# Kernel tuning notes

Measured on AMD Instinct MI355X. Metric: run time of the kernel, lower is better.

The kernel has to match this reference:

```python
import jax, jax.numpy as jnp
import numpy as np
from jax import lax

WINDOW = 11
C1 = (0.01 * 1) ** 2
C2 = (0.03 * 1) ** 2


def setup_inputs() -> dict:
    key = jax.random.key(0)
    kx, ky = jax.random.split(key)
    x = jax.random.uniform(kx, (8, 3, 512, 512), dtype=jnp.float32)
    y = jax.random.uniform(ky, (8, 3, 512, 512), dtype=jnp.float32)
    return {"x": x, "y": y}


def _window_sum(a):
    # sum over every overlapping WINDOW x WINDOW patch (stride 1, valid)
    return lax.reduce_window(a, 0.0, lax.add,
                             (1, 1, WINDOW, WINDOW),
                             (1, 1, 1, 1), 'VALID')


def reference(x, y):
    # x, y: [B, C, H, W] images in [0, 1]
    n = float(WINDOW * WINDOW)
    sx = _window_sum(x)
    sy = _window_sum(y)
    sxx = _window_sum(x * x)
    syy = _window_sum(y * y)
    sxy = _window_sum(x * y)
    mx = sx / n
    my = sy / n
    # unbiased variance / covariance (matches torch var(unbiased=True) and
    # the bessel-corrected covariance in the original)
    vx = (sxx - n * mx * mx) / (n - 1.0)
    vy = (syy - n * my * my) / (n - 1.0)
    cov = (sxy - n * mx * my) / (n - 1.0)
    ssim = (2.0 * mx * my + C1) * (2.0 * cov + C2) / (
        (mx * mx + my * my + C1) * (vx + vy + C2))
    # original averages over windows (dim 0) and channels (dim 2) -> per-batch
    return (1.0 - ssim.mean(axis=(1, 2, 3))) / 2.0
```

## Files before the change

kernel.cpp:

```cpp
#include <hip/hip_runtime.h>

#define WINDOW 11
#define H 512
#define W 512
#define OH 502
#define OW 502
#define NCH 3
#define BATCH 8
#define RSTRIPE 11
#define NSTRIPES 46
#define NGRP 5
#define GRPW 118
#define WAVES_PER_IMG (NSTRIPES * NGRP)
#define NWAVES (BATCH * NCH * WAVES_PER_IMG)
#define WAVES_PER_BATCH (NCH * WAVES_PER_IMG)
#define NXCD 8
#define CHUNK (NWAVES / NXCD)

#define NPIX_PER_BATCH (3.0f * 502.0f * 502.0f)

typedef float v2f __attribute__((ext_vector_type(2)));

template <int CTRL, int RM>
__device__ __forceinline__ float scan_step(float x) {
    int s = __builtin_amdgcn_update_dpp(0, __builtin_bit_cast(int, x),
                                        CTRL, RM, 0xf, false);
    return x + __builtin_bit_cast(float, s);
}
__device__ __forceinline__ float wave_iscan(float x) {
    x = scan_step<0x111, 0xf>(x);
    x = scan_step<0x112, 0xf>(x);
    x = scan_step<0x114, 0xf>(x);
    x = scan_step<0x118, 0xf>(x);
    x = scan_step<0x142, 0xa>(x);
    x = scan_step<0x143, 0xc>(x);
    return x;
}

__global__ __launch_bounds__(64) void ssim_main(const float* __restrict__ x,
                                                const float* __restrict__ y,
                                                float* __restrict__ partials) {
    const int lane = threadIdx.x & 63;

    const int wg    = blockIdx.x;
    const int w_lin = (wg % NXCD) * CHUNK + wg / NXCD;

    const int img = w_lin / WAVES_PER_IMG;
    const int rem = w_lin % WAVES_PER_IMG;
    const int grp = rem / NSTRIPES;
    const int rs  = rem % NSTRIPES;

    const int i0 = rs * RSTRIPE;
    const int i1 = min(i0 + RSTRIPE, OH);
    const int cstart = grp * GRPW;
    const int outw   = min(GRPW, OW - cstart);
    const int c0 = min(cstart + 2 * lane, W - 2);
    const bool tapActive = (2 * lane < outw);

    const float* __restrict__ xc = x + (size_t)img * H * W + c0;
    const float* __restrict__ yc = y + (size_t)img * H * W + c0;

    v2f fx[11], fy[11];
    v2f Qx = 0.f, Qy = 0.f, Qz = 0.f, Qw = 0.f;
#pragma unroll
    for (int r = 0; r < WINDOW; ++r) {
        v2f a = *(const v2f*)(xc + (size_t)(i0 + r) * W);
        v2f b = *(const v2f*)(yc + (size_t)(i0 + r) * W);
        fx[r] = a; fy[r] = b;
        Qx += a;
        Qy += b;
        Qz += a * a + b * b;
        Qw += a * b;
    }

    v2f nxA, nyA, nxB, nyB;
#define LDROW(j, nx, ny) do {                                        \
        int jc_ = min((j), H - 1);                                   \
        nx = *(const v2f*)(xc + (size_t)jc_ * W);                    \
        ny = *(const v2f*)(yc + (size_t)jc_ * W);                    \
    } while (0)

#define SLIDE(u, nx, ny) do {                                         \
        Qx += nx - fx[u];                                             \
        Qy += ny - fy[u];                                             \
        Qz += nx * nx + ny * ny - fx[u] * fx[u] - fy[u] * fy[u];      \
        Qw += nx * ny - fx[u] * fy[u];                                \
        fx[u] = nx; fy[u] = ny;                                       \
    } while (0)

    float acc = 0.f;

#define COMPUTE(rowActive) do {                                               \
        float Tx = Qx.x + Qx.y, Ty = Qy.x + Qy.y;                             \
        float Tz = Qz.x + Qz.y, Tw = Qw.x + Qw.y;                             \
        float Sx = wave_iscan(Tx), Sy = wave_iscan(Ty);                       \
        float Sz = wave_iscan(Tz), Sw = wave_iscan(Tw);                       \
        int src = lane + 5;                                                   \
        float Ax = __shfl(Sx, src, 64), Ay = __shfl(Sy, src, 64);             \
        float Az = __shfl(Sz, src, 64), Aw = __shfl(Sw, src, 64);             \
        float Bx = __shfl(Qx.y, src, 64), By = __shfl(Qy.y, src, 64);         \
        float Bz = __shfl(Qz.y, src, 64), Bw = __shfl(Qw.y, src, 64);         \
        v2f Wx = {Ax - Bx - Sx + Tx, Ax - Sx + Qx.y};                         \
        v2f Wy = {Ay - By - Sy + Ty, Ay - Sy + Qy.y};                         \
        v2f Wz = {Az - Bz - Sz + Tz, Az - Sz + Qz.y};                         \
        v2f Ww = {Aw - Bw - Sw + Tw, Aw - Sw + Qw.y};                         \
                             \
        v2f mx  = Wx * (1.0f / 121.0f);                                       \
        v2f my  = Wy * (1.0f / 121.0f);                                       \
        v2f mxy = mx * my;                                                    \
        v2f m2  = mx * mx + my * my;                                          \
        v2f cov = (Ww - 121.0f * mxy) * (1.0f / 120.0f);                      \
        v2f vv  = (Wz - 121.0f * m2)  * (1.0f / 120.0f);                      \
        v2f num = (2.0f * mxy + 1e-4f) * (2.0f * cov + 9e-4f);                \
        v2f den = (m2 + 1e-4f) * (vv + 9e-4f);                                \
        float r = num.x * __builtin_amdgcn_rcpf(den.x)                        \
                + num.y * __builtin_amdgcn_rcpf(den.y);                       \
        acc += (tapActive & (rowActive)) ? r : 0.f;                           \
    } while (0)

    LDROW(i0 + WINDOW,     nxA, nyA);
    LDROW(i0 + WINDOW + 1, nxB, nyB);
#pragma unroll
    for (int u = 0; u < 11; ++u) {
        const int i = i0 + u;
        COMPUTE(i < i1);
        if ((u & 1) == 0) {
            SLIDE(u, nxA, nyA);
            LDROW(i + WINDOW + 2, nxA, nyA);
        } else {
            SLIDE(u, nxB, nyB);
            LDROW(i + WINDOW + 2, nxB, nyB);
        }
    }

    for (int off = 32; off > 0; off >>= 1)
        acc += __shfl_down(acc, off, 64);
    if (lane == 0) partials[w_lin] = acc;
}

__global__ __launch_bounds__(64) void ssim_reduce(const float* __restrict__ partials,
                                                  float* __restrict__ out) {
    const int b    = blockIdx.x;
    const int lane = threadIdx.x & 63;
    float s = 0.f;
    for (int k = lane; k < WAVES_PER_BATCH; k += 64)
        s += partials[b * WAVES_PER_BATCH + k];
    for (int off = 32; off > 0; off >>= 1)
        s += __shfl_down(s, off, 64);
    if (lane == 0)
        out[b] = (1.0f - s / NPIX_PER_BATCH) * 0.5f;
}

extern "C" void kernel_launch(void* const* d_in, const int* in_sizes, int n_in,
                              void* d_out, int out_size, void* d_ws, size_t ws_size,
                              hipStream_t stream) {
    const float* x = (const float*)d_in[0];
    const float* y = (const float*)d_in[1];
    float* out      = (float*)d_out;
    float* partials = (float*)d_ws;

    ssim_main<<<NWAVES, 64, 0, stream>>>(x, y, partials);
    ssim_reduce<<<BATCH, 64, 0, stream>>>(partials, out);
}
```

Before: 29.60 us.

## Process full-width rows per wave with 8 columns per lane and 2-row stripes

Each wave now covers a whole 512-wide row, with every lane loading 8 contiguous columns as two float4 loads. A stripe is now 2 output rows instead of 11 rows across 5 column groups. Horizontal window sums use a local prefix plus a wave scan and shuffles from lanes +1 and +2. This removes the overlapping column-group halos and gives wider, coalesced loads. The cost is re-reading the 11-row vertical window for every 2 output rows, which is roughly 6x more vertical reload traffic (mostly cache hits), plus more waves and higher register use.

```diff
diff --git a/kernel.cpp b/kernel.cpp
--- a/kernel.cpp
+++ b/kernel.cpp
@@ -7,11 +7,9 @@
 #define OW 502
 #define NCH 3
 #define BATCH 8
-#define RSTRIPE 11
-#define NSTRIPES 46
-#define NGRP 5
-#define GRPW 118
-#define WAVES_PER_IMG (NSTRIPES * NGRP)
+#define RSTRIPE 2
+#define NSTRIPES 251
+#define WAVES_PER_IMG NSTRIPES
 #define NWAVES (BATCH * NCH * WAVES_PER_IMG)
 #define WAVES_PER_BATCH (NCH * WAVES_PER_IMG)
 #define NXCD 8
@@ -19,6 +17,7 @@
 
 #define NPIX_PER_BATCH (3.0f * 502.0f * 502.0f)
 
+typedef float v4f __attribute__((ext_vector_type(4)));
 typedef float v2f __attribute__((ext_vector_type(2)));
 
 template <int CTRL, int RM>
@@ -46,92 +45,110 @@
     const int w_lin = (wg % NXCD) * CHUNK + wg / NXCD;
 
     const int img = w_lin / WAVES_PER_IMG;
-    const int rem = w_lin % WAVES_PER_IMG;
-    const int grp = rem / NSTRIPES;
-    const int rs  = rem % NSTRIPES;
+    const int rs  = w_lin % WAVES_PER_IMG;
+    const int r0  = 2 * rs;
 
-    const int i0 = rs * RSTRIPE;
-    const int i1 = min(i0 + RSTRIPE, OH);
-    const int cstart = grp * GRPW;
-    const int outw   = min(GRPW, OW - cstart);
-    const int c0 = min(cstart + 2 * lane, W - 2);
-    const bool tapActive = (2 * lane < outw);
-
+    const int c0 = 8 * lane;
     const float* __restrict__ xc = x + (size_t)img * H * W + c0;
     const float* __restrict__ yc = y + (size_t)img * H * W + c0;
 
-    v2f fx[11], fy[11];
-    v2f Qx = 0.f, Qy = 0.f, Qz = 0.f, Qw = 0.f;
+    const bool mp0 = (c0     <= 500);
+    const bool mp1 = (c0 + 2 <= 500);
+    const bool mp2 = (c0 + 4 <= 500);
+    const bool mp3 = (c0 + 6 <= 500);
+
+    const int l1 = lane + 1, l2 = lane + 2;
+
+    v4f Qx0 = 0.f, Qx1 = 0.f, Qy0 = 0.f, Qy1 = 0.f;
+    v4f Qz0 = 0.f, Qz1 = 0.f, Qw0 = 0.f, Qw1 = 0.f;
+    v4f ka0, ka1, kb0, kb1;
+
+#define ACC(a0, a1, b0, b1) do {                                      \
+        Qx0 += a0; Qx1 += a1;                                         \
+        Qy0 += b0; Qy1 += b1;                                         \
+        Qz0 += a0 * a0 + b0 * b0; Qz1 += a1 * a1 + b1 * b1;           \
+        Qw0 += a0 * b0;           Qw1 += a1 * b1;                     \
+    } while (0)
+
 #pragma unroll
     for (int r = 0; r < WINDOW; ++r) {
-        v2f a = *(const v2f*)(xc + (size_t)(i0 + r) * W);
-        v2f b = *(const v2f*)(yc + (size_t)(i0 + r) * W);
-        fx[r] = a; fy[r] = b;
-        Qx += a;
-        Qy += b;
-        Qz += a * a + b * b;
-        Qw += a * b;
+        v4f a0 = *(const v4f*)(xc + (size_t)(r0 + r) * W);
+        v4f a1 = *(const v4f*)(xc + (size_t)(r0 + r) * W + 4);
+        v4f b0 = *(const v4f*)(yc + (size_t)(r0 + r) * W);
+        v4f b1 = *(const v4f*)(yc + (size_t)(r0 + r) * W + 4);
+        if (r == 0) { ka0 = a0; ka1 = a1; kb0 = b0; kb1 = b1; }
+        ACC(a0, a1, b0, b1);
     }
-
-    v2f nxA, nyA, nxB, nyB;
-#define LDROW(j, nx, ny) do {                                        \
-        int jc_ = min((j), H - 1);                                   \
-        nx = *(const v2f*)(xc + (size_t)jc_ * W);                    \
-        ny = *(const v2f*)(yc + (size_t)jc_ * W);                    \
-    } while (0)
-
-#define SLIDE(u, nx, ny) do {                                         \
-        Qx += nx - fx[u];                                             \
-        Qy += ny - fy[u];                                             \
-        Qz += nx * nx + ny * ny - fx[u] * fx[u] - fy[u] * fy[u];      \
-        Qw += nx * ny - fx[u] * fy[u];                                \
-        fx[u] = nx; fy[u] = ny;                                       \
-    } while (0)
 
     float acc = 0.f;
 
-#define COMPUTE(rowActive) do {                                               \
-        float Tx = Qx.x + Qx.y, Ty = Qy.x + Qy.y;                             \
-        float Tz = Qz.x + Qz.y, Tw = Qw.x + Qw.y;                             \
-        float Sx = wave_iscan(Tx), Sy = wave_iscan(Ty);                       \
-        float Sz = wave_iscan(Tz), Sw = wave_iscan(Tw);                       \
-        int src = lane + 5;                                                   \
-        float Ax = __shfl(Sx, src, 64), Ay = __shfl(Sy, src, 64);             \
-        float Az = __shfl(Sz, src, 64), Aw = __shfl(Sw, src, 64);             \
-        float Bx = __shfl(Qx.y, src, 64), By = __shfl(Qy.y, src, 64);         \
-        float Bz = __shfl(Qz.y, src, 64), Bw = __shfl(Qw.y, src, 64);         \
-        v2f Wx = {Ax - Bx - Sx + Tx, Ax - Sx + Qx.y};                         \
-        v2f Wy = {Ay - By - Sy + Ty, Ay - Sy + Qy.y};                         \
-        v2f Wz = {Az - Bz - Sz + Tz, Az - Sz + Qz.y};                         \
-        v2f Ww = {Aw - Bw - Sw + Tw, Aw - Sw + Qw.y};                         \
-                             \
-        v2f mx  = Wx * (1.0f / 121.0f);                                       \
-        v2f my  = Wy * (1.0f / 121.0f);                                       \
-        v2f mxy = mx * my;                                                    \
-        v2f m2  = mx * mx + my * my;                                          \
-        v2f cov = (Ww - 121.0f * mxy) * (1.0f / 120.0f);                      \
-        v2f vv  = (Wz - 121.0f * m2)  * (1.0f / 120.0f);                      \
-        v2f num = (2.0f * mxy + 1e-4f) * (2.0f * cov + 9e-4f);                \
-        v2f den = (m2 + 1e-4f) * (vv + 9e-4f);                                \
-        float r = num.x * __builtin_amdgcn_rcpf(den.x)                        \
-                + num.y * __builtin_amdgcn_rcpf(den.y);                       \
-        acc += (tapActive & (rowActive)) ? r : 0.f;                           \
+#define QWIN(Q0, Q1, w0, w1, w2, w3, w4, w5, w6, w7) do {             \
+        float p0 = Q0.x, p1 = p0 + Q0.y, p2 = p1 + Q0.z;              \
+        float p3 = p2 + Q0.w, p4 = p3 + Q1.x, p5 = p4 + Q1.y;         \
+        float p6 = p5 + Q1.z, T = p6 + Q1.w;                          \
+        float S = wave_iscan(T);                                      \
+        float E = S - T;                                              \
+        float s0 = E + p0, s1 = E + p1, s2 = E + p2, s3 = E + p3;     \
+        float s4 = E + p4, s5 = E + p5, s6 = E + p6;                  \
+        float r1s2 = __shfl(s2, l1, 64), r1s3 = __shfl(s3, l1, 64);   \
+        float r1s4 = __shfl(s4, l1, 64), r1s5 = __shfl(s5, l1, 64);   \
+        float r1s6 = __shfl(s6, l1, 64), r1s7 = __shfl(S,  l1, 64);   \
+        float r2s0 = __shfl(s0, l2, 64), r2s1 = __shfl(s1, l2, 64);   \
+        w0 = r1s2 - E;  w1 = r1s3 - s0;                               \
+        w2 = r1s4 - s1; w3 = r1s5 - s2;                               \
+        w4 = r1s6 - s3; w5 = r1s7 - s4;                               \
+        w6 = r2s0 - s5; w7 = r2s1 - s6;                               \
     } while (0)
 
-    LDROW(i0 + WINDOW,     nxA, nyA);
-    LDROW(i0 + WINDOW + 1, nxB, nyB);
-#pragma unroll
-    for (int u = 0; u < 11; ++u) {
-        const int i = i0 + u;
-        COMPUTE(i < i1);
-        if ((u & 1) == 0) {
-            SLIDE(u, nxA, nyA);
-            LDROW(i + WINDOW + 2, nxA, nyA);
-        } else {
-            SLIDE(u, nxB, nyB);
-            LDROW(i + WINDOW + 2, nxB, nyB);
-        }
+#define SSIM_PAIR(mask, WxP, WyP, WzP, WwP) do {                      \
+        v2f mx  = WxP * (1.0f / 121.0f);                              \
+        v2f my  = WyP * (1.0f / 121.0f);                              \
+        v2f mxy = mx * my;                                            \
+        v2f m2  = mx * mx + my * my;                                  \
+        v2f cov = (WwP - 121.0f * mxy) * (1.0f / 120.0f);             \
+        v2f vv  = (WzP - 121.0f * m2)  * (1.0f / 120.0f);             \
+        v2f num = (2.0f * mxy + 1e-4f) * (2.0f * cov + 9e-4f);        \
+        v2f den = (m2 + 1e-4f) * (vv + 9e-4f);                        \
+        float r = num.x * __builtin_amdgcn_rcpf(den.x)                \
+                + num.y * __builtin_amdgcn_rcpf(den.y);               \
+        acc += (mask) ? r : 0.f;                                      \
+    } while (0)
+
+#define COMPUTE() do {                                                        \
+        float wx0,wx1,wx2,wx3,wx4,wx5,wx6,wx7;                                \
+        float wy0,wy1,wy2,wy3,wy4,wy5,wy6,wy7;                                \
+        float wz0,wz1,wz2,wz3,wz4,wz5,wz6,wz7;                                \
+        float ww0,ww1,ww2,ww3,ww4,ww5,ww6,ww7;                                \
+        QWIN(Qx0,Qx1, wx0,wx1,wx2,wx3,wx4,wx5,wx6,wx7);                       \
+        QWIN(Qy0,Qy1, wy0,wy1,wy2,wy3,wy4,wy5,wy6,wy7);                       \
+        QWIN(Qz0,Qz1, wz0,wz1,wz2,wz3,wz4,wz5,wz6,wz7);                       \
+        QWIN(Qw0,Qw1, ww0,ww1,ww2,ww3,ww4,ww5,ww6,ww7);                       \
+        { v2f Wx={wx0,wx1}, Wy={wy0,wy1}, Wz={wz0,wz1}, Ww={ww0,ww1};         \
+          SSIM_PAIR(mp0, Wx, Wy, Wz, Ww); }                                   \
+        { v2f Wx={wx2,wx3}, Wy={wy2,wy3}, Wz={wz2,wz3}, Ww={ww2,ww3};         \
+          SSIM_PAIR(mp1, Wx, Wy, Wz, Ww); }                                   \
+        { v2f Wx={wx4,wx5}, Wy={wy4,wy5}, Wz={wz4,wz5}, Ww={ww4,ww5};         \
+          SSIM_PAIR(mp2, Wx, Wy, Wz, Ww); }                                   \
+        { v2f Wx={wx6,wx7}, Wy={wy6,wy7}, Wz={wz6,wz7}, Ww={ww6,ww7};         \
+          SSIM_PAIR(mp3, Wx, Wy, Wz, Ww); }                                   \
+    } while (0)
+
+    COMPUTE();
+
+    {
+        v4f na0 = *(const v4f*)(xc + (size_t)(r0 + WINDOW) * W);
+        v4f na1 = *(const v4f*)(xc + (size_t)(r0 + WINDOW) * W + 4);
+        v4f nb0 = *(const v4f*)(yc + (size_t)(r0 + WINDOW) * W);
+        v4f nb1 = *(const v4f*)(yc + (size_t)(r0 + WINDOW) * W + 4);
+        Qx0 += na0 - ka0; Qx1 += na1 - ka1;
+        Qy0 += nb0 - kb0; Qy1 += nb1 - kb1;
+        Qz0 += na0 * na0 + nb0 * nb0 - ka0 * ka0 - kb0 * kb0;
+        Qz1 += na1 * na1 + nb1 * nb1 - ka1 * ka1 - kb1 * kb1;
+        Qw0 += na0 * nb0 - ka0 * kb0;
+        Qw1 += na1 * nb1 - ka1 * kb1;
     }
+
+    COMPUTE();
 
     for (int off = 32; off > 0; off >>= 1)
         acc += __shfl_down(acc, off, 64);
```

Measured after the change: 27.33 us. 1.08x faster.

## Stage all stripe rows into LDS via async global_load_lds with staged waits

Applied to the files above, without the earlier changes.

Replaces the register-held sliding window of direct global v2f loads with asynchronous global-to-LDS loads of all 21 rows per stripe issued up front. Each row step then waits on a decreasing vmcnt and reads the new and old rows from LDS. The aim is to keep every load in flight at once and release register pressure from the fx/fy arrays. In exchange it adds LDS traffic, uses about 21KB of LDS per 64-thread block, which may limit occupancy, and relies on per-lane dword global_load_lds ordering semantics.

```diff
diff --git a/kernel.cpp b/kernel.cpp
--- a/kernel.cpp
+++ b/kernel.cpp
@@ -21,6 +21,17 @@
 
 typedef float v2f __attribute__((ext_vector_type(2)));
 
+#define GL_LDS(gsrc, ldst)                                                    \
+    __builtin_amdgcn_global_load_lds(                                         \
+        (const __attribute__((address_space(1))) unsigned int*)(gsrc),        \
+        (__attribute__((address_space(3))) unsigned int*)(ldst), 4, 0, 0)
+
+template <int N>
+__device__ __forceinline__ void vwait() {
+    asm volatile("s_waitcnt vmcnt(%0)" :: "i"(N) : "memory");
+    __builtin_amdgcn_sched_barrier(0);
+}
+
 template <int CTRL, int RM>
 __device__ __forceinline__ float scan_step(float x) {
     int s = __builtin_amdgcn_update_dpp(0, __builtin_bit_cast(int, x),
@@ -40,6 +51,9 @@
 __global__ __launch_bounds__(64) void ssim_main(const float* __restrict__ x,
                                                 const float* __restrict__ y,
                                                 float* __restrict__ partials) {
+    __shared__ float LX[21][128];
+    __shared__ float LY[21][128];
+
     const int lane = threadIdx.x & 63;
 
     const int wg    = blockIdx.x;
@@ -54,39 +68,24 @@
     const int i1 = min(i0 + RSTRIPE, OH);
     const int cstart = grp * GRPW;
     const int outw   = min(GRPW, OW - cstart);
-    const int c0 = min(cstart + 2 * lane, W - 2);
     const bool tapActive = (2 * lane < outw);
 
-    const float* __restrict__ xc = x + (size_t)img * H * W + c0;
-    const float* __restrict__ yc = y + (size_t)img * H * W + c0;
+    const float* __restrict__ xi = x + (size_t)img * H * W;
+    const float* __restrict__ yi = y + (size_t)img * H * W;
 
-    v2f fx[11], fy[11];
-    v2f Qx = 0.f, Qy = 0.f, Qz = 0.f, Qw = 0.f;
+    const int c_lo = min(cstart + lane, W - 1);
+    const int c_hi = min(cstart + 64 + lane, W - 1);
+
 #pragma unroll
-    for (int r = 0; r < WINDOW; ++r) {
-        v2f a = *(const v2f*)(xc + (size_t)(i0 + r) * W);
-        v2f b = *(const v2f*)(yc + (size_t)(i0 + r) * W);
-        fx[r] = a; fy[r] = b;
-        Qx += a;
-        Qy += b;
-        Qz += a * a + b * b;
-        Qw += a * b;
+    for (int r = 0; r < 21; ++r) {
+        const int row = min(i0 + r, H - 1);
+        const float* bx = xi + (size_t)row * W;
+        const float* by = yi + (size_t)row * W;
+        GL_LDS(bx + c_lo, &LX[r][0]);
+        GL_LDS(bx + c_hi, &LX[r][64]);
+        GL_LDS(by + c_lo, &LY[r][0]);
+        GL_LDS(by + c_hi, &LY[r][64]);
     }
-
-    v2f nxA, nyA, nxB, nyB;
-#define LDROW(j, nx, ny) do {                                        \
-        int jc_ = min((j), H - 1);                                   \
-        nx = *(const v2f*)(xc + (size_t)jc_ * W);                    \
-        ny = *(const v2f*)(yc + (size_t)jc_ * W);                    \
-    } while (0)
-
-#define SLIDE(u, nx, ny) do {                                         \
-        Qx += nx - fx[u];                                             \
-        Qy += ny - fy[u];                                             \
-        Qz += nx * nx + ny * ny - fx[u] * fx[u] - fy[u] * fy[u];      \
-        Qw += nx * ny - fx[u] * fy[u];                                \
-        fx[u] = nx; fy[u] = ny;                                       \
-    } while (0)
 
     float acc = 0.f;
 
@@ -104,7 +103,6 @@
         v2f Wy = {Ay - By - Sy + Ty, Ay - Sy + Qy.y};                         \
         v2f Wz = {Az - Bz - Sz + Tz, Az - Sz + Qz.y};                         \
         v2f Ww = {Aw - Bw - Sw + Tw, Aw - Sw + Qw.y};                         \
-                             \
         v2f mx  = Wx * (1.0f / 121.0f);                                       \
         v2f my  = Wy * (1.0f / 121.0f);                                       \
         v2f mxy = mx * my;                                                    \
@@ -118,20 +116,34 @@
         acc += (tapActive & (rowActive)) ? r : 0.f;                           \
     } while (0)
 
-    LDROW(i0 + WINDOW,     nxA, nyA);
-    LDROW(i0 + WINDOW + 1, nxB, nyB);
+    vwait<40>();
+    v2f Qx = 0.f, Qy = 0.f, Qz = 0.f, Qw = 0.f;
 #pragma unroll
-    for (int u = 0; u < 11; ++u) {
-        const int i = i0 + u;
-        COMPUTE(i < i1);
-        if ((u & 1) == 0) {
-            SLIDE(u, nxA, nyA);
-            LDROW(i + WINDOW + 2, nxA, nyA);
-        } else {
-            SLIDE(u, nxB, nyB);
-            LDROW(i + WINDOW + 2, nxB, nyB);
-        }
+    for (int r = 0; r < WINDOW; ++r) {
+        v2f a = *(const v2f*)&LX[r][2 * lane];
+        v2f b = *(const v2f*)&LY[r][2 * lane];
+        Qx += a;
+        Qy += b;
+        Qz += a * a + b * b;
+        Qw += a * b;
     }
+    COMPUTE(true);
+
+#define STEP(U, N) do {                                               \
+        vwait<N>();                                                   \
+        v2f nx = *(const v2f*)&LX[11 + (U)][2 * lane];                \
+        v2f ny = *(const v2f*)&LY[11 + (U)][2 * lane];                \
+        v2f ox = *(const v2f*)&LX[(U)][2 * lane];                     \
+        v2f oy = *(const v2f*)&LY[(U)][2 * lane];                     \
+        Qx += nx - ox;                                                \
+        Qy += ny - oy;                                                \
+        Qz += nx * nx + ny * ny - ox * ox - oy * oy;                  \
+        Qw += nx * ny - ox * oy;                                      \
+        COMPUTE(i0 + (U) + 1 < i1);                                   \
+    } while (0)
+
+    STEP(0, 36); STEP(1, 32); STEP(2, 28); STEP(3, 24); STEP(4, 20);
+    STEP(5, 16); STEP(6, 12); STEP(7, 8);  STEP(8, 4);  STEP(9, 0);
 
     for (int off = 32; off > 0; off >>= 1)
         acc += __shfl_down(acc, off, 64);
```

Result: slower. 35.66 us (+20.5%).
